# Kernel tuning notes

Hardware: AMD Instinct MI355X
Metric: run time of the kernel (lower is better)

Reference implementation:

```python
import jax, jax.numpy as jnp
import numpy as np

B, C, CI, H, W = 8, 256, 128, 64, 64
STD = 0.01  # conv_init_std
EPS = 1e-5


def setup_inputs() -> dict:
    key = jax.random.key(0)
    ks = jax.random.split(key, 6)
    return {
        "x": jax.random.normal(ks[0], (B, C, H, W), dtype=jnp.float32),
        "theta_w": jax.random.normal(ks[1], (CI, C), dtype=jnp.float32) * STD,
        "theta_b": jnp.zeros((CI,), jnp.float32),
        "phi_w": jax.random.normal(ks[2], (CI, C), dtype=jnp.float32) * STD,
        "phi_b": jnp.zeros((CI,), jnp.float32),
        "g_w": jax.random.normal(ks[3], (CI, C), dtype=jnp.float32) * STD,
        "g_b": jnp.zeros((CI,), jnp.float32),
        "wz_w": jax.random.normal(ks[4], (C, CI), dtype=jnp.float32) * STD,
        "wz_b": jnp.zeros((C,), jnp.float32),
        "bn_gamma": jnp.ones((C,), jnp.float32),
        "bn_beta": jnp.zeros((C,), jnp.float32),
    }


def _conv1x1(x, w, b):
    # 1x1 conv == channel matmul: (B,Cin,H,W),(Cout,Cin) -> (B,Cout,H,W)
    return jnp.einsum('bchw,oc->bohw', x, w) + b[None, :, None, None]


def reference(x, theta_w, theta_b, phi_w, phi_b, g_w, g_b, wz_w, wz_b, bn_gamma, bn_beta):
    b, c, h, w = x.shape
    ci = theta_w.shape[0]
    # query over full resolution: (B, CI, N) with N = H*W
    theta = _conv1x1(x, theta_w, theta_b).reshape(b, ci, h * w)
    # 2x2 maxpool stride 2 for key/value inputs
    xp = x.reshape(b, c, h // 2, 2, w // 2, 2).max(axis=(3, 5))
    phi = _conv1x1(xp, phi_w, phi_b).reshape(b, ci, -1)   # (B, CI, N')
    g = _conv1x1(xp, g_w, g_b).reshape(b, ci, -1)         # (B, CI, N')
    # scaled dot-product attention: scores (B, N, N')
    scores = jnp.einsum('bcn,bcm->bnm', theta, phi) * (ci ** -0.5)
    p = jax.nn.softmax(scores, axis=-1)
    t = jnp.einsum('bcm,bnm->bcn', g, p).reshape(b, ci, h, w)
    z = _conv1x1(t, wz_w, wz_b)
    # BatchNorm2d, training-mode batch statistics (biased variance)
    mean = z.mean(axis=(0, 2, 3))
    var = z.var(axis=(0, 2, 3))
    z = (z - mean[None, :, None, None]) * jax.lax.rsqrt(var + EPS)[None, :, None, None]
    z = z * bn_gamma[None, :, None, None] + bn_beta[None, :, None, None]
    return x + z
```

## Files before the change

kernel.cpp:

```cpp
#include <hip/hip_runtime.h>

#define B_   8
#define C_   256
#define CI_  128
#define HW_  4096
#define HWP_ 1024

typedef short bf16x8 __attribute__((ext_vector_type(8)));
typedef float f32x4 __attribute__((ext_vector_type(4)));
typedef unsigned short u16;
typedef unsigned int u32;

#define SW(row, off) ((off) ^ (((row) & 7) << 4))

__device__ __forceinline__ u16 f2b(float f) {
  u32 u = __builtin_bit_cast(u32, f);
  return (u16)((u + 0x7fffu + ((u >> 16) & 1u)) >> 16);
}

__device__ __forceinline__ f32x4 mfma16(bf16x8 a, bf16x8 b, f32x4 c) {
  return __builtin_amdgcn_mfma_f32_16x16x32_bf16(a, b, c, 0, 0, 0);
}

__global__ __launch_bounds__(256) void prep(const float* __restrict__ x,
                                            u16* __restrict__ xt,
                                            u16* __restrict__ xpt) {
  __shared__ __align__(16) char sm[16384];
  const int b = blockIdx.z, c0 = blockIdx.y * 64, p = blockIdx.x;
  const int t = threadIdx.x;
#pragma unroll
  for (int k = 0; k < 2; ++k) {
    int pi = k * 256 + t;
    int ng = pi & 31, cg = pi >> 5;
    float4 v[4];
#pragma unroll
    for (int cc = 0; cc < 4; ++cc)
      v[cc] = *(const float4*)&x[((size_t)(b * C_ + c0 + cg * 4 + cc)) * HW_ + p * 128 + ng * 4];
#pragma unroll
    for (int jj = 0; jj < 4; ++jj) {
      int n = ng * 4 + jj;
      uint2 pk;
      pk.x = (u32)f2b(v[0][jj]) | ((u32)f2b(v[1][jj]) << 16);
      pk.y = (u32)f2b(v[2][jj]) | ((u32)f2b(v[3][jj]) << 16);
      int slot = (cg + ng) & 15;
      *(uint2*)(sm + n * 128 + slot * 8) = pk;
    }
  }
  __syncthreads();
#pragma unroll
  for (int it = 0; it < 4; ++it) {
    int L = it * 256 + t;
    int row = L >> 3, ch = L & 7;
    int s0 = (2 * ch + (row >> 2)) & 15, s1 = (2 * ch + 1 + (row >> 2)) & 15;
    uint2 a = *(const uint2*)(sm + row * 128 + s0 * 8);
    uint2 bb = *(const uint2*)(sm + row * 128 + s1 * 8);
    uint4 o = {a.x, a.y, bb.x, bb.y};
    *(uint4*)(xt + ((size_t)(b * HW_ + p * 128 + row)) * C_ + c0 + ch * 8) = o;
  }
#pragma unroll
  for (int k = 0; k < 2; ++k) {
    int cg = t & 15, mw = (t >> 4) + k * 16;
    int rows[4] = {2 * mw, 2 * mw + 1, 64 + 2 * mw, 65 + 2 * mw};
    uint2 rv[4];
#pragma unroll
    for (int r = 0; r < 4; ++r) {
      int n = rows[r];
      int slot = (cg + (n >> 2)) & 15;
      rv[r] = *(const uint2*)(sm + n * 128 + slot * 8);
    }
    u16 outc[4];
#pragma unroll
    for (int ci = 0; ci < 4; ++ci) {
      float m = -1e30f;
#pragma unroll
      for (int r = 0; r < 4; ++r) {
        u32 word = (ci < 2) ? rv[r].x : rv[r].y;
        u16 h = (u16)((ci & 1) ? (word >> 16) : (word & 0xffff));
        m = fmaxf(m, __builtin_bit_cast(float, (u32)h << 16));
      }
      outc[ci] = (u16)(__builtin_bit_cast(u32, m) >> 16);
    }
    uint2 pk;
    pk.x = (u32)outc[0] | ((u32)outc[1] << 16);
    pk.y = (u32)outc[2] | ((u32)outc[3] << 16);
    *(uint2*)(xpt + ((size_t)(b * HWP_ + p * 32 + mw)) * C_ + c0 + cg * 4) = pk;
  }
}

__global__ __launch_bounds__(256) void gemm_wa(const float* __restrict__ Wf,
                                               const u16* __restrict__ act,
                                               const float* __restrict__ bias,
                                               u16* __restrict__ outp,
                                               int Ntok) {
  __shared__ __align__(16) char smem[32768];
  char* Ws = smem;
  char* Xs = smem + 16384;
  const int b = blockIdx.y;
  const int n0 = blockIdx.x * 128;
  const int t = threadIdx.x, l = t & 63, w = t >> 6;
  const int lr = l & 15, lg = l >> 4;
  const int otb = (w & 1) * 4, ntb = (w >> 1) * 4;
  f32x4 acc[4][4];
#pragma unroll
  for (int i = 0; i < 4; ++i)
#pragma unroll
    for (int j = 0; j < 4; ++j) acc[i][j] = (f32x4){0.f, 0.f, 0.f, 0.f};

  for (int kc = 0; kc < 4; ++kc) {
    __syncthreads();
#pragma unroll
    for (int it = 0; it < 4; ++it) {
      int L = it * 256 + t;
      int row = L >> 3, ch = L & 7;
      const float* src = Wf + (size_t)row * 256 + kc * 64 + ch * 8;
      float4 f0 = *(const float4*)src;
      float4 f1 = *(const float4*)(src + 4);
      uint4 v;
      v.x = (u32)f2b(f0.x) | ((u32)f2b(f0.y) << 16);
      v.y = (u32)f2b(f0.z) | ((u32)f2b(f0.w) << 16);
      v.z = (u32)f2b(f1.x) | ((u32)f2b(f1.y) << 16);
      v.w = (u32)f2b(f1.z) | ((u32)f2b(f1.w) << 16);
      *(uint4*)(Ws + row * 128 + SW(row, ch * 16)) = v;
    }
#pragma unroll
    for (int it = 0; it < 4; ++it) {
      int L = it * 256 + t;
      int row = L >> 3, ch = L & 7;
      uint4 v = *(const uint4*)(act + ((size_t)b * Ntok + n0 + row) * 256 + kc * 64 + ch * 8);
      *(uint4*)(Xs + row * 128 + SW(row, ch * 16)) = v;
    }
    __syncthreads();
#pragma unroll
    for (int ks = 0; ks < 2; ++ks) {
      bf16x8 af[4], bfr[4];
#pragma unroll
      for (int i = 0; i < 4; ++i) {
        int rA = (otb + i) * 16 + lr;
        af[i] = *(const bf16x8*)(Ws + rA * 128 + SW(rA, ks * 64 + lg * 16));
        int rB = (ntb + i) * 16 + lr;
        bfr[i] = *(const bf16x8*)(Xs + rB * 128 + SW(rB, ks * 64 + lg * 16));
      }
#pragma unroll
      for (int i = 0; i < 4; ++i)
#pragma unroll
        for (int j = 0; j < 4; ++j) acc[i][j] = mfma16(af[i], bfr[j], acc[i][j]);
    }
  }
  __syncthreads();
#pragma unroll
  for (int i = 0; i < 4; ++i) {
    int obase = (otb + i) * 16 + lg * 4;
    float b0 = bias[obase], b1 = bias[obase + 1], b2 = bias[obase + 2], b3 = bias[obase + 3];
#pragma unroll
    for (int j = 0; j < 4; ++j) {
      int n = (ntb + j) * 16 + lr;
      f32x4 v = acc[i][j];
      uint2 pk;
      pk.x = (u32)f2b(v[0] + b0) | ((u32)f2b(v[1] + b1) << 16);
      pk.y = (u32)f2b(v[2] + b2) | ((u32)f2b(v[3] + b3) << 16);
      *(uint2*)(smem + n * 256 + SW(n, obase * 2)) = pk;
    }
  }
  __syncthreads();
#pragma unroll
  for (int it = 0; it < 8; ++it) {
    int L = it * 256 + t;
    int row = L >> 4, ch = L & 15;
    uint4 v = *(const uint4*)(smem + row * 256 + SW(row, ch * 16));
    *(uint4*)(outp + ((size_t)b * Ntok + n0 + row) * 128 + ch * 8) = v;
  }
}

template <int KD, bool F32OUT, bool BNP>
__global__ __launch_bounds__(256) void gemm_aw(const u16* __restrict__ act,
                                               const float* __restrict__ Wf,
                                               const float* __restrict__ bias,
                                               void* __restrict__ outp,
                                               int Mtok, int O,
                                               float* __restrict__ sums,
                                               float* __restrict__ sqs) {
  __shared__ __align__(16) char smem[32768];
  char* As = smem;
  char* Bs = smem + 8192;
  const int b = blockIdx.z;
  const int m0 = blockIdx.x * 64;
  const int o0 = blockIdx.y * 128;
  const int t = threadIdx.x, l = t & 63, w = t >> 6;
  const int lr = l & 15, lg = l >> 4;
  const int otb = w * 2;
  f32x4 acc[4][2];
#pragma unroll
  for (int i = 0; i < 4; ++i)
#pragma unroll
    for (int j = 0; j < 2; ++j) acc[i][j] = (f32x4){0.f, 0.f, 0.f, 0.f};

  for (int kc = 0; kc < KD / 64; ++kc) {
    __syncthreads();
#pragma unroll
    for (int it = 0; it < 2; ++it) {
      int L = it * 256 + t;
      int row = L >> 3, ch = L & 7;
      uint4 v = *(const uint4*)(act + ((size_t)b * Mtok + m0 + row) * KD + kc * 64 + ch * 8);
      *(uint4*)(As + row * 128 + SW(row, ch * 16)) = v;
    }
#pragma unroll
    for (int it = 0; it < 4; ++it) {
      int L = it * 256 + t;
      int row = L >> 3, ch = L & 7;
      const float* src = Wf + (size_t)(o0 + row) * KD + kc * 64 + ch * 8;
      float4 f0 = *(const float4*)src;
      float4 f1 = *(const float4*)(src + 4);
      uint4 v;
      v.x = (u32)f2b(f0.x) | ((u32)f2b(f0.y) << 16);
      v.y = (u32)f2b(f0.z) | ((u32)f2b(f0.w) << 16);
      v.z = (u32)f2b(f1.x) | ((u32)f2b(f1.y) << 16);
      v.w = (u32)f2b(f1.z) | ((u32)f2b(f1.w) << 16);
      *(uint4*)(Bs + row * 128 + SW(row, ch * 16)) = v;
    }
    __syncthreads();
#pragma unroll
    for (int ks = 0; ks < 2; ++ks) {
      bf16x8 af[4], bfr[2];
#pragma unroll
      for (int i = 0; i < 4; ++i) {
        int r = i * 16 + lr;
        af[i] = *(const bf16x8*)(As + r * 128 + SW(r, ks * 64 + lg * 16));
      }
#pragma unroll
      for (int j = 0; j < 2; ++j) {
        int r = (otb + j) * 16 + lr;
        bfr[j] = *(const bf16x8*)(Bs + r * 128 + SW(r, ks * 64 + lg * 16));
      }
#pragma unroll
      for (int i = 0; i < 4; ++i)
#pragma unroll
        for (int j = 0; j < 2; ++j) acc[i][j] = mfma16(af[i], bfr[j], acc[i][j]);
    }
  }
  if (BNP) {
    int pid = blockIdx.z * gridDim.x + blockIdx.x;
#pragma unroll
    for (int j = 0; j < 2; ++j) {
      int o = o0 + (otb + j) * 16 + lr;
      float bi = bias[o];
      float s = 0.f, q = 0.f;
#pragma unroll
      for (int i = 0; i < 4; ++i) {
        f32x4 v = acc[i][j];
#pragma unroll
        for (int r = 0; r < 4; ++r) {
          float vv = v[r] + bi;
          s += vv;
          q += vv * vv;
        }
      }
      s += __shfl_xor(s, 16); q += __shfl_xor(q, 16);
      s += __shfl_xor(s, 32); q += __shfl_xor(q, 32);
      if (lg == 0) {
        sums[(size_t)o * 512 + pid] = s;
        sqs[(size_t)o * 512 + pid] = q;
      }
    }
  }
  __syncthreads();
#pragma unroll
  for (int j = 0; j < 2; ++j) {
    int o = (otb + j) * 16 + lr;
    float bi = bias[o0 + o];
#pragma unroll
    for (int i = 0; i < 4; ++i) {
      int mq = i * 16 + lg * 4;
      f32x4 v = acc[i][j];
      if (F32OUT) {
        f32x4 vb = {v[0] + bi, v[1] + bi, v[2] + bi, v[3] + bi};
        *(f32x4*)(smem + o * 256 + SW(o, mq * 4)) = vb;
      } else {
        uint2 pk;
        pk.x = (u32)f2b(v[0] + bi) | ((u32)f2b(v[1] + bi) << 16);
        pk.y = (u32)f2b(v[2] + bi) | ((u32)f2b(v[3] + bi) << 16);
        *(uint2*)(smem + o * 128 + SW(o, mq * 2)) = pk;
      }
    }
  }
  __syncthreads();
  if (F32OUT) {
    float* dst = (float*)outp;
#pragma unroll
    for (int it = 0; it < 8; ++it) {
      int L = it * 256 + t;
      int row = L >> 4, ch = L & 15;
      uint4 v = *(const uint4*)(smem + row * 256 + SW(row, ch * 16));
      *(uint4*)(dst + ((size_t)b * O + o0 + row) * Mtok + m0 + ch * 4) = v;
    }
  } else {
    u16* dst = (u16*)outp;
#pragma unroll
    for (int it = 0; it < 4; ++it) {
      int L = it * 256 + t;
      int row = L >> 3, ch = L & 7;
      uint4 v = *(const uint4*)(smem + row * 128 + SW(row, ch * 16));
      *(uint4*)(dst + ((size_t)b * O + o0 + row) * Mtok + m0 + ch * 8) = v;
    }
  }
}

__global__ __launch_bounds__(256) void attn_mfma(const u16* __restrict__ Qt,
                                                 const u16* __restrict__ Kt,
                                                 const u16* __restrict__ Vn,
                                                 u16* __restrict__ Ot) {
  __shared__ __align__(16) char smem[57344];
  char* Qs = smem;
  char* Ks = smem + 16384;
  char* Vs = smem + 32768;
  char* Pn = smem + 49152;
  const int bid = blockIdx.x;
  const int swz = (bid & 7) * 64 + (bid >> 3);
  const int b = swz >> 6, n0 = (swz & 63) * 64;
  const int t = threadIdx.x, l = t & 63, w = t >> 6;
  const int lr = l & 15, lg = l >> 4;
  const float scale = 0.08838834764831845f;

#pragma unroll
  for (int it = 0; it < 4; ++it) {
    int L = it * 256 + t;
    int row = L >> 4, ch = L & 15;
    uint4 v = *(const uint4*)(Qt + ((size_t)b * HW_ + n0 + row) * 128 + ch * 8);
    *(uint4*)(Qs + row * 256 + SW(row, ch * 16)) = v;
  }
  __syncthreads();
  bf16x8 qf[4];
  {
    int r = w * 16 + lr;
#pragma unroll
    for (int kc = 0; kc < 4; ++kc)
      qf[kc] = *(const bf16x8*)(Qs + r * 256 + SW(r, kc * 64 + lg * 16));
  }
  f32x4 accT[8];
#pragma unroll
  for (int ct = 0; ct < 8; ++ct) accT[ct] = (f32x4){0.f, 0.f, 0.f, 0.f};
  float csum = 0.f;

  for (int m0 = 0; m0 < HWP_; m0 += 64) {
    __syncthreads();
#pragma unroll
    for (int it = 0; it < 4; ++it) {
      int L = it * 256 + t;
      int row = L >> 4, ch = L & 15;
      uint4 v = *(const uint4*)(Kt + ((size_t)b * HWP_ + m0 + row) * 128 + ch * 8);
      *(uint4*)(Ks + row * 256 + SW(row, ch * 16)) = v;
    }
#pragma unroll
    for (int it = 0; it < 4; ++it) {
      int L = it * 256 + t;
      int row = L >> 3, ch = L & 7;
      uint4 v = *(const uint4*)(Vn + ((size_t)b * 128 + row) * HWP_ + m0 + ch * 8);
      *(uint4*)(Vs + row * 128 + SW(row, ch * 16)) = v;
    }
    __syncthreads();
    int rn = w * 16 + lr;
#pragma unroll
    for (int mt = 0; mt < 4; ++mt) {
      f32x4 s = {0.f, 0.f, 0.f, 0.f};
#pragma unroll
      for (int kc = 0; kc < 4; ++kc) {
        int r = mt * 16 + lr;
        bf16x8 a = *(const bf16x8*)(Ks + r * 256 + SW(r, kc * 64 + lg * 16));
        s = mfma16(a, qf[kc], s);
      }
      float p0 = __expf(s[0] * scale), p1 = __expf(s[1] * scale);
      float p2 = __expf(s[2] * scale), p3 = __expf(s[3] * scale);
      csum += (p0 + p1) + (p2 + p3);
      uint2 pk;
      pk.x = (u32)f2b(p0) | ((u32)f2b(p1) << 16);
      pk.y = (u32)f2b(p2) | ((u32)f2b(p3) << 16);
      *(uint2*)(Pn + rn * 128 + SW(rn, mt * 32 + lg * 8)) = pk;
    }
    asm volatile("s_waitcnt lgkmcnt(0)" ::: "memory");
    bf16x8 pb0 = *(const bf16x8*)(Pn + rn * 128 + SW(rn, lg * 16));
    bf16x8 pb1 = *(const bf16x8*)(Pn + rn * 128 + SW(rn, 64 + lg * 16));
#pragma unroll
    for (int ct = 0; ct < 8; ++ct) {
      int rc = ct * 16 + lr;
      bf16x8 a0 = *(const bf16x8*)(Vs + rc * 128 + SW(rc, lg * 16));
      bf16x8 a1 = *(const bf16x8*)(Vs + rc * 128 + SW(rc, 64 + lg * 16));
      accT[ct] = mfma16(a0, pb0, accT[ct]);
      accT[ct] = mfma16(a1, pb1, accT[ct]);
    }
  }
  csum += __shfl_xor(csum, 16);
  csum += __shfl_xor(csum, 32);
  float rinv = 1.f / csum;
  __syncthreads();
  {
    int rn = w * 16 + lr;
#pragma unroll
    for (int ct = 0; ct < 8; ++ct) {
      f32x4 v = accT[ct];
      uint2 pk;
      pk.x = (u32)f2b(v[0] * rinv) | ((u32)f2b(v[1] * rinv) << 16);
      pk.y = (u32)f2b(v[2] * rinv) | ((u32)f2b(v[3] * rinv) << 16);
      *(uint2*)(Ks + rn * 256 + SW(rn, ct * 32 + lg * 8)) = pk;
    }
  }
  __syncthreads();
#pragma unroll
  for (int it = 0; it < 4; ++it) {
    int L = it * 256 + t;
    int row = L >> 4, ch = L & 15;
    uint4 v = *(const uint4*)(Ks + row * 256 + SW(row, ch * 16));
    *(uint4*)(Ot + ((size_t)b * HW_ + n0 + row) * 128 + ch * 8) = v;
  }
}

__global__ __launch_bounds__(256) void bn_finalize(const float* __restrict__ sums,
                                                   const float* __restrict__ sqs,
                                                   float* __restrict__ stats) {
  __shared__ float s1[256], s2[256];
  const int c = blockIdx.x, t = threadIdx.x;
  float a = sums[(size_t)c * 512 + t] + sums[(size_t)c * 512 + 256 + t];
  float q = sqs[(size_t)c * 512 + t] + sqs[(size_t)c * 512 + 256 + t];
  s1[t] = a;
  s2[t] = q;
  __syncthreads();
  for (int st = 128; st > 0; st >>= 1) {
    if (t < st) {
      s1[t] += s1[t + st];
      s2[t] += s2[t + st];
    }
    __syncthreads();
  }
  if (t == 0) {
    const float inv = 1.f / (float)(B_ * HW_);
    float mean = s1[0] * inv;
    float var = s2[0] * inv - mean * mean;
    stats[c] = mean;
    stats[C_ + c] = rsqrtf(var + 1e-5f);
  }
}

__global__ __launch_bounds__(256) void final4(const float4* __restrict__ x,
                                              const float4* __restrict__ z,
                                              const float* __restrict__ stats,
                                              const float* __restrict__ gamma,
                                              const float* __restrict__ beta,
                                              float4* __restrict__ out) {
  size_t i = (size_t)blockIdx.x * 256 + threadIdx.x;
  int c = (int)((i >> 10) & 255);
  float mean = stats[c], istd = stats[C_ + c];
  float ga = gamma[c] * istd, be = beta[c] - mean * ga;
  float4 xv = x[i], zv = z[i], o;
  o.x = xv.x + zv.x * ga + be;
  o.y = xv.y + zv.y * ga + be;
  o.z = xv.z + zv.z * ga + be;
  o.w = xv.w + zv.w * ga + be;
  out[i] = o;
}

extern "C" void kernel_launch(void* const* d_in, const int* in_sizes, int n_in,
                              void* d_out, int out_size, void* d_ws, size_t ws_size,
                              hipStream_t stream) {
  const float* x        = (const float*)d_in[0];
  const float* theta_w  = (const float*)d_in[1];
  const float* theta_b  = (const float*)d_in[2];
  const float* phi_w    = (const float*)d_in[3];
  const float* phi_b    = (const float*)d_in[4];
  const float* g_w      = (const float*)d_in[5];
  const float* g_b      = (const float*)d_in[6];
  const float* wz_w     = (const float*)d_in[7];
  const float* wz_b     = (const float*)d_in[8];
  const float* bn_gamma = (const float*)d_in[9];
  const float* bn_beta  = (const float*)d_in[10];
  float* out = (float*)d_out;

  char* ws = (char*)d_ws;
  u16* x_t     = (u16*)(ws);
  u16* xp_t    = (u16*)(ws + 16777216);
  u16* theta_t = (u16*)(ws + 20971520);
  u16* phi_t   = (u16*)(ws + 29360128);
  u16* g_nat   = (u16*)(ws + 31457280);
  u16* t_t     = (u16*)(ws + 33554432);
  float* z     = (float*)(ws + 41943040);
  float* stats = (float*)(ws + 75497472);
  float* bsums = (float*)(ws + 75499520);
  float* bsqs  = (float*)(ws + 76023808);

  prep<<<dim3(32, 4, 8), 256, 0, stream>>>(x, x_t, xp_t);
  gemm_wa<<<dim3(32, 8), 256, 0, stream>>>(theta_w, x_t, theta_b, theta_t, HW_);
  gemm_wa<<<dim3(8, 8), 256, 0, stream>>>(phi_w, xp_t, phi_b, phi_t, HWP_);
  gemm_aw<256, false, false><<<dim3(16, 1, 8), 256, 0, stream>>>(
      xp_t, g_w, g_b, g_nat, HWP_, 128, nullptr, nullptr);
  attn_mfma<<<dim3(512), 256, 0, stream>>>(theta_t, phi_t, g_nat, t_t);
  gemm_aw<128, true, true><<<dim3(64, 2, 8), 256, 0, stream>>>(
      t_t, wz_w, wz_b, z, HW_, 256, bsums, bsqs);
  bn_finalize<<<256, 256, 0, stream>>>(bsums, bsqs, stats);
  final4<<<8192, 256, 0, stream>>>((const float4*)x, (const float4*)z, stats,
                                   bn_gamma, bn_beta, (float4*)out);
}
```

Baseline: 190.6 us.

## Pre-convert weights to bf16, async LDS double-buffering, bf16 z intermediate

Weights are converted to bf16 once in extra prep blocks rather than on every GEMM tile load. The GEMMs and attention now stage tiles with global_load_lds, double-buffered so the next chunk loads while the current one computes. The conv output z is stored as bf16 instead of fp32, which halves its write and read traffic in the final BN-residual kernel. The manual bf16 rounding is replaced by the hardware v_cvt_pk_bf16_f32 instruction. The cost is extra LDS per block, which may reduce occupancy, and lower precision in z before normalization.

```diff
diff --git a/kernel.cpp b/kernel.cpp
--- a/kernel.cpp
+++ b/kernel.cpp
@@ -17,17 +17,70 @@
   u32 u = __builtin_bit_cast(u32, f);
   return (u16)((u + 0x7fffu + ((u >> 16) & 1u)) >> 16);
 }
-
+__device__ __forceinline__ u32 cvtpk(float lo, float hi) {
+  u32 r;
+  asm("v_cvt_pk_bf16_f32 %0, %1, %2" : "=v"(r) : "v"(lo), "v"(hi));
+  return r;
+}
 __device__ __forceinline__ f32x4 mfma16(bf16x8 a, bf16x8 b, f32x4 c) {
   return __builtin_amdgcn_mfma_f32_16x16x32_bf16(a, b, c, 0, 0, 0);
 }
+__device__ __forceinline__ void gl16(const void* g, void* l) {
+  __builtin_amdgcn_global_load_lds(
+      (const __attribute__((address_space(1))) u32*)g,
+      (__attribute__((address_space(3))) u32*)l, 16, 0, 0);
+}
+
+template <int ROWS>
+__device__ __forceinline__ void stage_tile(const u16* src, int rstride,
+                                           char* lds, int w, int lane) {
+#pragma unroll
+  for (int it = 0; it < ROWS / 32; ++it) {
+    int L = it * 256 + w * 64 + lane;
+    int row = L >> 3, slot = L & 7;
+    gl16(src + (size_t)row * rstride + ((slot ^ (row & 7)) << 3),
+         lds + it * 4096 + w * 1024);
+  }
+}
+__device__ __forceinline__ void stage_tile256(const u16* src, char* lds, int w, int lane) {
+#pragma unroll
+  for (int it = 0; it < 4; ++it) {
+    int L = it * 256 + w * 64 + lane;
+    int row = L >> 4, slot = L & 15;
+    gl16(src + (size_t)row * 128 + ((slot ^ (row & 7)) << 3),
+         lds + it * 4096 + w * 1024);
+  }
+}
 
 __global__ __launch_bounds__(256) void prep(const float* __restrict__ x,
                                             u16* __restrict__ xt,
-                                            u16* __restrict__ xpt) {
+                                            u16* __restrict__ xpt,
+                                            const float* __restrict__ w0,
+                                            const float* __restrict__ w1,
+                                            const float* __restrict__ w2,
+                                            const float* __restrict__ w3,
+                                            u16* __restrict__ wB) {
+  const int b = blockIdx.z, p = blockIdx.x;
+  const int t = threadIdx.x;
+  if (p == 32) {
+    if (blockIdx.y == 0 && b < 4) {
+      const float* src = (b == 0) ? w0 : (b == 1) ? w1 : (b == 2) ? w2 : w3;
+      u16* dst = wB + b * 32768;
+      for (int i = t * 8; i < 32768; i += 2048) {
+        float4 a = *(const float4*)&src[i];
+        float4 c = *(const float4*)&src[i + 4];
+        uint4 v;
+        v.x = cvtpk(a.x, a.y);
+        v.y = cvtpk(a.z, a.w);
+        v.z = cvtpk(c.x, c.y);
+        v.w = cvtpk(c.z, c.w);
+        *(uint4*)&dst[i] = v;
+      }
+    }
+    return;
+  }
   __shared__ __align__(16) char sm[16384];
-  const int b = blockIdx.z, c0 = blockIdx.y * 64, p = blockIdx.x;
-  const int t = threadIdx.x;
+  const int c0 = blockIdx.y * 64;
 #pragma unroll
   for (int k = 0; k < 2; ++k) {
     int pi = k * 256 + t;
@@ -40,8 +93,8 @@
     for (int jj = 0; jj < 4; ++jj) {
       int n = ng * 4 + jj;
       uint2 pk;
-      pk.x = (u32)f2b(v[0][jj]) | ((u32)f2b(v[1][jj]) << 16);
-      pk.y = (u32)f2b(v[2][jj]) | ((u32)f2b(v[3][jj]) << 16);
+      pk.x = cvtpk(v[0][jj], v[1][jj]);
+      pk.y = cvtpk(v[2][jj], v[3][jj]);
       int slot = (cg + ng) & 15;
       *(uint2*)(sm + n * 128 + slot * 8) = pk;
     }
@@ -87,49 +140,35 @@
   }
 }
 
-__global__ __launch_bounds__(256) void gemm_wa(const float* __restrict__ Wf,
+__global__ __launch_bounds__(256) void gemm_wa(const u16* __restrict__ Wb,
                                                const u16* __restrict__ act,
                                                const float* __restrict__ bias,
                                                u16* __restrict__ outp,
                                                int Ntok) {
-  __shared__ __align__(16) char smem[32768];
-  char* Ws = smem;
-  char* Xs = smem + 16384;
+  __shared__ __align__(16) char smem[65536];
   const int b = blockIdx.y;
   const int n0 = blockIdx.x * 128;
-  const int t = threadIdx.x, l = t & 63, w = t >> 6;
-  const int lr = l & 15, lg = l >> 4;
+  const int t = threadIdx.x, lane = t & 63, w = t >> 6;
+  const int lr = lane & 15, lg = lane >> 4;
   const int otb = (w & 1) * 4, ntb = (w >> 1) * 4;
+  const u16* actb = act + (size_t)(b * Ntok + n0) * 256;
   f32x4 acc[4][4];
 #pragma unroll
   for (int i = 0; i < 4; ++i)
 #pragma unroll
     for (int j = 0; j < 4; ++j) acc[i][j] = (f32x4){0.f, 0.f, 0.f, 0.f};
 
+  stage_tile<128>(Wb, 256, smem, w, lane);
+  stage_tile<128>(actb, 256, smem + 16384, w, lane);
   for (int kc = 0; kc < 4; ++kc) {
     __syncthreads();
-#pragma unroll
-    for (int it = 0; it < 4; ++it) {
-      int L = it * 256 + t;
-      int row = L >> 3, ch = L & 7;
-      const float* src = Wf + (size_t)row * 256 + kc * 64 + ch * 8;
-      float4 f0 = *(const float4*)src;
-      float4 f1 = *(const float4*)(src + 4);
-      uint4 v;
-      v.x = (u32)f2b(f0.x) | ((u32)f2b(f0.y) << 16);
-      v.y = (u32)f2b(f0.z) | ((u32)f2b(f0.w) << 16);
-      v.z = (u32)f2b(f1.x) | ((u32)f2b(f1.y) << 16);
-      v.w = (u32)f2b(f1.z) | ((u32)f2b(f1.w) << 16);
-      *(uint4*)(Ws + row * 128 + SW(row, ch * 16)) = v;
-    }
-#pragma unroll
-    for (int it = 0; it < 4; ++it) {
-      int L = it * 256 + t;
-      int row = L >> 3, ch = L & 7;
-      uint4 v = *(const uint4*)(act + ((size_t)b * Ntok + n0 + row) * 256 + kc * 64 + ch * 8);
-      *(uint4*)(Xs + row * 128 + SW(row, ch * 16)) = v;
-    }
-    __syncthreads();
+    if (kc < 3) {
+      char* nb = smem + ((kc + 1) & 1) * 32768;
+      stage_tile<128>(Wb + (kc + 1) * 64, 256, nb, w, lane);
+      stage_tile<128>(actb + (kc + 1) * 64, 256, nb + 16384, w, lane);
+    }
+    char* Ws = smem + (kc & 1) * 32768;
+    char* Xs = Ws + 16384;
 #pragma unroll
     for (int ks = 0; ks < 2; ++ks) {
       bf16x8 af[4], bfr[4];
@@ -146,7 +185,6 @@
         for (int j = 0; j < 4; ++j) acc[i][j] = mfma16(af[i], bfr[j], acc[i][j]);
     }
   }
-  __syncthreads();
 #pragma unroll
   for (int i = 0; i < 4; ++i) {
     int obase = (otb + i) * 16 + lg * 4;
@@ -156,8 +194,8 @@
       int n = (ntb + j) * 16 + lr;
       f32x4 v = acc[i][j];
       uint2 pk;
-      pk.x = (u32)f2b(v[0] + b0) | ((u32)f2b(v[1] + b1) << 16);
-      pk.y = (u32)f2b(v[2] + b2) | ((u32)f2b(v[3] + b3) << 16);
+      pk.x = cvtpk(v[0] + b0, v[1] + b1);
+      pk.y = cvtpk(v[2] + b2, v[3] + b3);
       *(uint2*)(smem + n * 256 + SW(n, obase * 2)) = pk;
     }
   }
@@ -171,53 +209,41 @@
   }
 }
 
-template <int KD, bool F32OUT, bool BNP>
+template <int KD, bool BNP>
 __global__ __launch_bounds__(256) void gemm_aw(const u16* __restrict__ act,
-                                               const float* __restrict__ Wf,
+                                               const u16* __restrict__ Wb,
                                                const float* __restrict__ bias,
-                                               void* __restrict__ outp,
+                                               u16* __restrict__ outp,
                                                int Mtok, int O,
                                                float* __restrict__ sums,
                                                float* __restrict__ sqs) {
-  __shared__ __align__(16) char smem[32768];
-  char* As = smem;
-  char* Bs = smem + 8192;
+  __shared__ __align__(16) char smem[49152];
   const int b = blockIdx.z;
   const int m0 = blockIdx.x * 64;
   const int o0 = blockIdx.y * 128;
-  const int t = threadIdx.x, l = t & 63, w = t >> 6;
-  const int lr = l & 15, lg = l >> 4;
+  const int t = threadIdx.x, lane = t & 63, w = t >> 6;
+  const int lr = lane & 15, lg = lane >> 4;
   const int otb = w * 2;
+  const u16* actb = act + (size_t)(b * Mtok + m0) * KD;
+  const u16* Wbb = Wb + (size_t)o0 * KD;
+  constexpr int NCH = KD / 64;
   f32x4 acc[4][2];
 #pragma unroll
   for (int i = 0; i < 4; ++i)
 #pragma unroll
     for (int j = 0; j < 2; ++j) acc[i][j] = (f32x4){0.f, 0.f, 0.f, 0.f};
 
-  for (int kc = 0; kc < KD / 64; ++kc) {
+  stage_tile<64>(actb, KD, smem, w, lane);
+  stage_tile<128>(Wbb, KD, smem + 8192, w, lane);
+  for (int kc = 0; kc < NCH; ++kc) {
     __syncthreads();
-#pragma unroll
-    for (int it = 0; it < 2; ++it) {
-      int L = it * 256 + t;
-      int row = L >> 3, ch = L & 7;
-      uint4 v = *(const uint4*)(act + ((size_t)b * Mtok + m0 + row) * KD + kc * 64 + ch * 8);
-      *(uint4*)(As + row * 128 + SW(row, ch * 16)) = v;
-    }
-#pragma unroll
-    for (int it = 0; it < 4; ++it) {
-      int L = it * 256 + t;
-      int row = L >> 3, ch = L & 7;
-      const float* src = Wf + (size_t)(o0 + row) * KD + kc * 64 + ch * 8;
-      float4 f0 = *(const float4*)src;
-      float4 f1 = *(const float4*)(src + 4);
-      uint4 v;
-      v.x = (u32)f2b(f0.x) | ((u32)f2b(f0.y) << 16);
-      v.y = (u32)f2b(f0.z) | ((u32)f2b(f0.w) << 16);
-      v.z = (u32)f2b(f1.x) | ((u32)f2b(f1.y) << 16);
-      v.w = (u32)f2b(f1.z) | ((u32)f2b(f1.w) << 16);
-      *(uint4*)(Bs + row * 128 + SW(row, ch * 16)) = v;
-    }
-    __syncthreads();
+    if (kc < NCH - 1) {
+      char* nb = smem + ((kc + 1) & 1) * 24576;
+      stage_tile<64>(actb + (kc + 1) * 64, KD, nb, w, lane);
+      stage_tile<128>(Wbb + (kc + 1) * 64, KD, nb + 8192, w, lane);
+    }
+    char* As = smem + (kc & 1) * 24576;
+    char* Bs = As + 8192;
 #pragma unroll
     for (int ks = 0; ks < 2; ++ks) {
       bf16x8 af[4], bfr[2];
@@ -262,7 +288,6 @@
       }
     }
   }
-  __syncthreads();
 #pragma unroll
   for (int j = 0; j < 2; ++j) {
     int o = (otb + j) * 16 + lr;
@@ -271,143 +296,121 @@
     for (int i = 0; i < 4; ++i) {
       int mq = i * 16 + lg * 4;
       f32x4 v = acc[i][j];
-      if (F32OUT) {
-        f32x4 vb = {v[0] + bi, v[1] + bi, v[2] + bi, v[3] + bi};
-        *(f32x4*)(smem + o * 256 + SW(o, mq * 4)) = vb;
-      } else {
-        uint2 pk;
-        pk.x = (u32)f2b(v[0] + bi) | ((u32)f2b(v[1] + bi) << 16);
-        pk.y = (u32)f2b(v[2] + bi) | ((u32)f2b(v[3] + bi) << 16);
-        *(uint2*)(smem + o * 128 + SW(o, mq * 2)) = pk;
-      }
-    }
-  }
-  __syncthreads();
-  if (F32OUT) {
-    float* dst = (float*)outp;
-#pragma unroll
-    for (int it = 0; it < 8; ++it) {
-      int L = it * 256 + t;
-      int row = L >> 4, ch = L & 15;
-      uint4 v = *(const uint4*)(smem + row * 256 + SW(row, ch * 16));
-      *(uint4*)(dst + ((size_t)b * O + o0 + row) * Mtok + m0 + ch * 4) = v;
-    }
-  } else {
-    u16* dst = (u16*)outp;
-#pragma unroll
-    for (int it = 0; it < 4; ++it) {
-      int L = it * 256 + t;
-      int row = L >> 3, ch = L & 7;
-      uint4 v = *(const uint4*)(smem + row * 128 + SW(row, ch * 16));
-      *(uint4*)(dst + ((size_t)b * O + o0 + row) * Mtok + m0 + ch * 8) = v;
-    }
-  }
-}
+      uint2 pk;
+      pk.x = cvtpk(v[0] + bi, v[1] + bi);
+      pk.y = cvtpk(v[2] + bi, v[3] + bi);
+      *(uint2*)(smem + o * 128 + SW(o, mq * 2)) = pk;
+    }
+  }
+  __syncthreads();
+#pragma unroll
+  for (int it = 0; it < 4; ++it) {
+    int L = it * 256 + t;
+    int row = L >> 3, ch = L & 7;
+    uint4 v = *(const uint4*)(smem + row * 128 + SW(row, ch * 16));
+    *(uint4*)(outp + ((size_t)b * O + o0 + row) * Mtok + m0 + ch * 8) = v;
+  }
+}
+
+#define ATTN_TILE(KCP, WAITV)                                                 \
+  {                                                                           \
+    const char* Kc = (KCP);                                                   \
+    int rn = w * 16 + lr;                                                     \
+    _Pragma("unroll")                                                         \
+    for (int mt = 0; mt < 4; ++mt) {                                          \
+      f32x4 s = {0.f, 0.f, 0.f, 0.f};                                         \
+      _Pragma("unroll")                                                       \
+      for (int kq = 0; kq < 4; ++kq) {                                        \
+        int r = mt * 16 + lr;                                                 \
+        bf16x8 a = *(const bf16x8*)(Kc + r * 256 + SW(r, kq * 64 + lg * 16)); \
+        s = mfma16(a, qf[kq], s);                                             \
+      }                                                                       \
+      float p0 = __expf(s[0] * scale), p1 = __expf(s[1] * scale);             \
+      float p2 = __expf(s[2] * scale), p3 = __expf(s[3] * scale);             \
+      csum += (p0 + p1) + (p2 + p3);                                          \
+      uint2 pk;                                                               \
+      pk.x = cvtpk(p0, p1);                                                   \
+      pk.y = cvtpk(p2, p3);                                                   \
+      *(uint2*)(Pn + rn * 128 + SW(rn, mt * 32 + lg * 8)) = pk;               \
+    }                                                                         \
+    asm volatile("s_waitcnt lgkmcnt(0)" ::: "memory");                        \
+    bf16x8 pb0 = *(const bf16x8*)(Pn + rn * 128 + SW(rn, lg * 16));           \
+    bf16x8 pb1 = *(const bf16x8*)(Pn + rn * 128 + SW(rn, 64 + lg * 16));      \
+    asm volatile("s_waitcnt " WAITV ::: "memory");                            \
+    _Pragma("unroll")                                                         \
+    for (int ct = 0; ct < 8; ++ct) {                                          \
+      int rc = ct * 16 + lr;                                                  \
+      bf16x8 a0 = *(const bf16x8*)(Vs + rc * 128 + SW(rc, lg * 16));          \
+      bf16x8 a1 = *(const bf16x8*)(Vs + rc * 128 + SW(rc, 64 + lg * 16));     \
+      accT[ct] = mfma16(a0, pb0, accT[ct]);                                   \
+      accT[ct] = mfma16(a1, pb1, accT[ct]);                                   \
+    }                                                                         \
+  }
 
 __global__ __launch_bounds__(256) void attn_mfma(const u16* __restrict__ Qt,
                                                  const u16* __restrict__ Kt,
                                                  const u16* __restrict__ Vn,
                                                  u16* __restrict__ Ot) {
-  __shared__ __align__(16) char smem[57344];
-  char* Qs = smem;
-  char* Ks = smem + 16384;
-  char* Vs = smem + 32768;
-  char* Pn = smem + 49152;
+  __shared__ __align__(16) char smem[73728];
+  char* Vs = smem + 49152;
+  char* Pn = smem + 65536;
   const int bid = blockIdx.x;
   const int swz = (bid & 7) * 64 + (bid >> 3);
   const int b = swz >> 6, n0 = (swz & 63) * 64;
-  const int t = threadIdx.x, l = t & 63, w = t >> 6;
-  const int lr = l & 15, lg = l >> 4;
+  const int t = threadIdx.x, lane = t & 63, w = t >> 6;
+  const int lr = lane & 15, lg = lane >> 4;
   const float scale = 0.08838834764831845f;
-
+  const u16* Qbase = Qt + (size_t)(b * HW_ + n0) * 128;
+  const u16* Kbase = Kt + (size_t)b * HWP_ * 128;
+  const u16* Vbase = Vn + (size_t)b * 128 * HWP_;
+
+  stage_tile256(Qbase, smem, w, lane);
+  stage_tile256(Kbase, smem + 16384, w, lane);
+  stage_tile<128>(Vbase, HWP_, Vs, w, lane);
+  __syncthreads();
+
+  bf16x8 qf[4];
+  {
+    int r = w * 16 + lr;
+#pragma unroll
+    for (int kq = 0; kq < 4; ++kq)
+      qf[kq] = *(const bf16x8*)(smem + r * 256 + SW(r, kq * 64 + lg * 16));
+  }
+  f32x4 accT[8];
+#pragma unroll
+  for (int ct = 0; ct < 8; ++ct) accT[ct] = (f32x4){0.f, 0.f, 0.f, 0.f};
+  float csum = 0.f;
+
+  for (int tt = 0; tt < 15; ++tt) {
+    stage_tile256(Kbase + (size_t)(tt + 1) * 64 * 128,
+                  smem + 16384 + ((tt + 1) & 1) * 16384, w, lane);
+    ATTN_TILE(smem + 16384 + (tt & 1) * 16384, "vmcnt(4)");
+    __syncthreads();
+    stage_tile<128>(Vbase + (tt + 1) * 64, HWP_, Vs, w, lane);
+  }
+  ATTN_TILE(smem + 16384 + 16384, "vmcnt(0)");
+
+  csum += __shfl_xor(csum, 16);
+  csum += __shfl_xor(csum, 32);
+  float rinv = 1.f / csum;
+  __syncthreads();
+  {
+    int rn = w * 16 + lr;
+#pragma unroll
+    for (int ct = 0; ct < 8; ++ct) {
+      f32x4 v = accT[ct];
+      uint2 pk;
+      pk.x = cvtpk(v[0] * rinv, v[1] * rinv);
+      pk.y = cvtpk(v[2] * rinv, v[3] * rinv);
+      *(uint2*)(smem + 16384 + rn * 256 + SW(rn, ct * 32 + lg * 8)) = pk;
+    }
+  }
+  __syncthreads();
 #pragma unroll
   for (int it = 0; it < 4; ++it) {
     int L = it * 256 + t;
     int row = L >> 4, ch = L & 15;
-    uint4 v = *(const uint4*)(Qt + ((size_t)b * HW_ + n0 + row) * 128 + ch * 8);
-    *(uint4*)(Qs + row * 256 + SW(row, ch * 16)) = v;
-  }
-  __syncthreads();
-  bf16x8 qf[4];
-  {
-    int r = w * 16 + lr;
-#pragma unroll
-    for (int kc = 0; kc < 4; ++kc)
-      qf[kc] = *(const bf16x8*)(Qs + r * 256 + SW(r, kc * 64 + lg * 16));
-  }
-  f32x4 accT[8];
-#pragma unroll
-  for (int ct = 0; ct < 8; ++ct) accT[ct] = (f32x4){0.f, 0.f, 0.f, 0.f};
-  float csum = 0.f;
-
-  for (int m0 = 0; m0 < HWP_; m0 += 64) {
-    __syncthreads();
-#pragma unroll
-    for (int it = 0; it < 4; ++it) {
-      int L = it * 256 + t;
-      int row = L >> 4, ch = L & 15;
-      uint4 v = *(const uint4*)(Kt + ((size_t)b * HWP_ + m0 + row) * 128 + ch * 8);
-      *(uint4*)(Ks + row * 256 + SW(row, ch * 16)) = v;
-    }
-#pragma unroll
-    for (int it = 0; it < 4; ++it) {
-      int L = it * 256 + t;
-      int row = L >> 3, ch = L & 7;
-      uint4 v = *(const uint4*)(Vn + ((size_t)b * 128 + row) * HWP_ + m0 + ch * 8);
-      *(uint4*)(Vs + row * 128 + SW(row, ch * 16)) = v;
-    }
-    __syncthreads();
-    int rn = w * 16 + lr;
-#pragma unroll
-    for (int mt = 0; mt < 4; ++mt) {
-      f32x4 s = {0.f, 0.f, 0.f, 0.f};
-#pragma unroll
-      for (int kc = 0; kc < 4; ++kc) {
-        int r = mt * 16 + lr;
-        bf16x8 a = *(const bf16x8*)(Ks + r * 256 + SW(r, kc * 64 + lg * 16));
-        s = mfma16(a, qf[kc], s);
-      }
-      float p0 = __expf(s[0] * scale), p1 = __expf(s[1] * scale);
-      float p2 = __expf(s[2] * scale), p3 = __expf(s[3] * scale);
-      csum += (p0 + p1) + (p2 + p3);
-      uint2 pk;
-      pk.x = (u32)f2b(p0) | ((u32)f2b(p1) << 16);
-      pk.y = (u32)f2b(p2) | ((u32)f2b(p3) << 16);
-      *(uint2*)(Pn + rn * 128 + SW(rn, mt * 32 + lg * 8)) = pk;
-    }
-    asm volatile("s_waitcnt lgkmcnt(0)" ::: "memory");
-    bf16x8 pb0 = *(const bf16x8*)(Pn + rn * 128 + SW(rn, lg * 16));
-    bf16x8 pb1 = *(const bf16x8*)(Pn + rn * 128 + SW(rn, 64 + lg * 16));
-#pragma unroll
-    for (int ct = 0; ct < 8; ++ct) {
-      int rc = ct * 16 + lr;
-      bf16x8 a0 = *(const bf16x8*)(Vs + rc * 128 + SW(rc, lg * 16));
-      bf16x8 a1 = *(const bf16x8*)(Vs + rc * 128 + SW(rc, 64 + lg * 16));
-      accT[ct] = mfma16(a0, pb0, accT[ct]);
-      accT[ct] = mfma16(a1, pb1, accT[ct]);
-    }
-  }
-  csum += __shfl_xor(csum, 16);
-  csum += __shfl_xor(csum, 32);
-  float rinv = 1.f / csum;
-  __syncthreads();
-  {
-    int rn = w * 16 + lr;
-#pragma unroll
-    for (int ct = 0; ct < 8; ++ct) {
-      f32x4 v = accT[ct];
-      uint2 pk;
-      pk.x = (u32)f2b(v[0] * rinv) | ((u32)f2b(v[1] * rinv) << 16);
-      pk.y = (u32)f2b(v[2] * rinv) | ((u32)f2b(v[3] * rinv) << 16);
-      *(uint2*)(Ks + rn * 256 + SW(rn, ct * 32 + lg * 8)) = pk;
-    }
-  }
-  __syncthreads();
-#pragma unroll
-  for (int it = 0; it < 4; ++it) {
-    int L = it * 256 + t;
-    int row = L >> 4, ch = L & 15;
-    uint4 v = *(const uint4*)(Ks + row * 256 + SW(row, ch * 16));
+    uint4 v = *(const uint4*)(smem + 16384 + row * 256 + SW(row, ch * 16));
     *(uint4*)(Ot + ((size_t)b * HW_ + n0 + row) * 128 + ch * 8) = v;
   }
 }
@@ -438,22 +441,31 @@
   }
 }
 
-__global__ __launch_bounds__(256) void final4(const float4* __restrict__ x,
-                                              const float4* __restrict__ z,
+__device__ __forceinline__ float blo(u32 u) { return __builtin_bit_cast(float, u << 16); }
+__device__ __forceinline__ float bhi(u32 u) { return __builtin_bit_cast(float, u & 0xffff0000u); }
+
+__global__ __launch_bounds__(256) void final8(const float4* __restrict__ x,
+                                              const uint4* __restrict__ zb,
                                               const float* __restrict__ stats,
                                               const float* __restrict__ gamma,
                                               const float* __restrict__ beta,
                                               float4* __restrict__ out) {
   size_t i = (size_t)blockIdx.x * 256 + threadIdx.x;
-  int c = (int)((i >> 10) & 255);
-  float mean = stats[c], istd = stats[C_ + c];
-  float ga = gamma[c] * istd, be = beta[c] - mean * ga;
-  float4 xv = x[i], zv = z[i], o;
-  o.x = xv.x + zv.x * ga + be;
-  o.y = xv.y + zv.y * ga + be;
-  o.z = xv.z + zv.z * ga + be;
-  o.w = xv.w + zv.w * ga + be;
-  out[i] = o;
+  int c = (int)((i >> 9) & 255);
+  float ga = gamma[c] * stats[C_ + c];
+  float be = beta[c] - stats[c] * ga;
+  uint4 zv = zb[i];
+  float4 x0 = x[2 * i], x1 = x[2 * i + 1], o0, o1;
+  o0.x = fmaf(blo(zv.x), ga, x0.x + be);
+  o0.y = fmaf(bhi(zv.x), ga, x0.y + be);
+  o0.z = fmaf(blo(zv.y), ga, x0.z + be);
+  o0.w = fmaf(bhi(zv.y), ga, x0.w + be);
+  o1.x = fmaf(blo(zv.z), ga, x1.x + be);
+  o1.y = fmaf(bhi(zv.z), ga, x1.y + be);
+  o1.z = fmaf(blo(zv.w), ga, x1.z + be);
+  o1.w = fmaf(bhi(zv.w), ga, x1.w + be);
+  out[2 * i] = o0;
+  out[2 * i + 1] = o1;
 }
 
 extern "C" void kernel_launch(void* const* d_in, const int* in_sizes, int n_in,
@@ -479,20 +491,21 @@
   u16* phi_t   = (u16*)(ws + 29360128);
   u16* g_nat   = (u16*)(ws + 31457280);
   u16* t_t     = (u16*)(ws + 33554432);
-  float* z     = (float*)(ws + 41943040);
-  float* stats = (float*)(ws + 75497472);
-  float* bsums = (float*)(ws + 75499520);
-  float* bsqs  = (float*)(ws + 76023808);
-
-  prep<<<dim3(32, 4, 8), 256, 0, stream>>>(x, x_t, xp_t);
-  gemm_wa<<<dim3(32, 8), 256, 0, stream>>>(theta_w, x_t, theta_b, theta_t, HW_);
-  gemm_wa<<<dim3(8, 8), 256, 0, stream>>>(phi_w, xp_t, phi_b, phi_t, HWP_);
-  gemm_aw<256, false, false><<<dim3(16, 1, 8), 256, 0, stream>>>(
-      xp_t, g_w, g_b, g_nat, HWP_, 128, nullptr, nullptr);
+  u16* zb      = (u16*)(ws + 41943040);
+  float* stats = (float*)(ws + 58720256);
+  float* bsums = (float*)(ws + 58722304);
+  float* bsqs  = (float*)(ws + 59246592);
+  u16* wB      = (u16*)(ws + 59770880);
+
+  prep<<<dim3(33, 4, 8), 256, 0, stream>>>(x, x_t, xp_t, theta_w, phi_w, g_w, wz_w, wB);
+  gemm_wa<<<dim3(32, 8), 256, 0, stream>>>(wB, x_t, theta_b, theta_t, HW_);
+  gemm_wa<<<dim3(8, 8), 256, 0, stream>>>(wB + 32768, xp_t, phi_b, phi_t, HWP_);
+  gemm_aw<256, false><<<dim3(16, 1, 8), 256, 0, stream>>>(
+      xp_t, wB + 65536, g_b, g_nat, HWP_, 128, nullptr, nullptr);
   attn_mfma<<<dim3(512), 256, 0, stream>>>(theta_t, phi_t, g_nat, t_t);
-  gemm_aw<128, true, true><<<dim3(64, 2, 8), 256, 0, stream>>>(
-      t_t, wz_w, wz_b, z, HW_, 256, bsums, bsqs);
+  gemm_aw<128, true><<<dim3(64, 2, 8), 256, 0, stream>>>(
+      t_t, wB + 98304, wz_b, zb, HW_, 256, bsums, bsqs);
   bn_finalize<<<256, 256, 0, stream>>>(bsums, bsqs, stats);
-  final4<<<8192, 256, 0, stream>>>((const float4*)x, (const float4*)z, stats,
+  final8<<<4096, 256, 0, stream>>>((const float4*)x, (const uint4*)zb, stats,
                                    bn_gamma, bn_beta, (float4*)out);
 }
```

New measurement: 169.1 us. 1.13x faster.
